# Kernel optimization log

Measured on AMD Instinct MI355X. Metric: run time of the kernel, lower is better.

Reference implementation:

```python
import jax, jax.numpy as jnp
import numpy as np

EPS = 1e-06


def setup_inputs() -> dict:
    key = jax.random.key(0)
    ks = jax.random.split(key, 8)
    B, N, D, r, T, O, Hid = 32, 2048, 64, 32, 31, 12, 128
    in_dim = r + T  # 63
    xav = lambda k, shape: jax.random.uniform(k, shape, jnp.float32, -1.0, 1.0) * np.sqrt(6.0 / (shape[0] + shape[1]))
    return {
        "H": jax.random.normal(ks[0], (B, N, D), jnp.float32),
        "ts_out": jax.random.uniform(ks[1], (B, O, T), jnp.float32),
        "O": O,
        "P_raw": xav(ks[2], (N, r)),
        "Q_raw": xav(ks[3], (N, r)),
        "W1": xav(ks[4], (in_dim, Hid)),
        "b1": jnp.zeros((Hid,), jnp.float32),
        "W2": xav(ks[5], (Hid, r)),
        "b2": jnp.zeros((r,), jnp.float32),
        "alpha": jax.random.uniform(ks[6], (1,), jnp.float32),
    }


def reference(H, ts_out, O, P_raw, Q_raw, W1, b1, W2, b2, alpha):
    # nonnegative_basis=True -> softplus on both bases
    P = jax.nn.softplus(P_raw)  # [N, r]
    Q = jax.nn.softplus(Q_raw)  # [N, r]
    # Right contraction: U = Q^T H per batch -> [B, r, D]
    U = jnp.einsum('bnd,nr->brd', H, Q)
    # Context norm over feature dim: [B, r]
    ctx = jnp.sqrt(jnp.mean(U * U, axis=-1) + EPS)
    # Gate features: concat([ts_out [B,O,T], ctx broadcast to [B,O,r]])
    B = H.shape[0]
    ctx_exp = jnp.broadcast_to(ctx[:, None, :], (B, O, ctx.shape[-1]))
    feat = jnp.concatenate([ts_out, ctx_exp], axis=-1)  # [B, O, T+r]
    # scale MLP with exact (erf) GELU, dropout=0 (eval)
    h = jax.nn.gelu(feat @ W1 + b1, approximate=False)
    s = jax.nn.softplus(h @ W2 + b2)  # [B, O, r]
    # M = P (s \odot U) without materializing NxN: [B, O, N, D]
    M = jnp.einsum('bor,brd,nr->bond', s, U, P)
    a = jnp.clip(alpha[0], 0.0, 1.0)
    H_base = H[:, None, :, :]  # broadcast over O
    H_graph = H_base + a * (M - H_base)
    return H_graph
```

## Files before the change

kernel.cpp:

```cpp
#include <hip/hip_runtime.h>
#include <math.h>

#define B_ 32
#define N_ 2048
#define D_ 64
#define R_ 32
#define T_ 31
#define O_ 12
#define HID_ 128
#define IN_DIM_ 63
#define NCH_ 32

#define OFF_QSP   0
#define OFF_UPART (OFF_QSP + N_*R_)
#define OFF_U     (OFF_UPART + B_*NCH_*R_*D_)
#define OFF_CTX   (OFF_U + B_*R_*D_)
#define OFF_PBF   (OFF_CTX + B_*R_)
#define OFF_SUT   (OFF_PBF + N_*R_/2)

typedef __attribute__((ext_vector_type(4))) float f32x4;
typedef __attribute__((ext_vector_type(8))) short short8;

__device__ __forceinline__ float softplus_f(float x) {
    return fmaxf(x, 0.0f) + log1pf(expf(-fabsf(x)));
}
__device__ __forceinline__ float gelu_f(float x) {
    return 0.5f * x * (1.0f + erff(x * 0.70710678118654752440f));
}
__device__ __forceinline__ unsigned short f2bf(float f) {
    unsigned int u = __float_as_uint(f);
    u = (u + 0x7FFFu + ((u >> 16) & 1u)) >> 16;
    return (unsigned short)u;
}

__global__ __launch_bounds__(256) void k_softplus(const float* __restrict__ Qr,
                                                  float* __restrict__ ws) {
    int i = blockIdx.x * blockDim.x + threadIdx.x;
    if (i < N_ * R_) ws[OFF_QSP + i] = softplus_f(Qr[i]);
}

__global__ __launch_bounds__(512) void k_upart(const float* __restrict__ H,
                                               const float* __restrict__ Pr,
                                               float* __restrict__ ws) {
    const float* __restrict__ Qsp = ws + OFF_QSP;
    float* __restrict__ Upart = ws + OFF_UPART;
    int b = blockIdx.x / NCH_;
    int c = blockIdx.x % NCH_;
    int tid = threadIdx.x;
    const int n0 = c * (N_ / NCH_);

    if (b == 0) {
        unsigned short* Pbf = (unsigned short*)(ws + OFF_PBF);
        #pragma unroll
        for (int i = tid; i < 64 * R_; i += 512)
            Pbf[(size_t)n0 * R_ + i] = f2bf(softplus_f(Pr[(size_t)n0 * R_ + i]));
    }

    int d = tid & 63;
    int rb = __builtin_amdgcn_readfirstlane(tid >> 6);
    const int r0 = rb * 4;
    float acc0 = 0.f, acc1 = 0.f, acc2 = 0.f, acc3 = 0.f;
    const float* __restrict__ Hb = H + ((size_t)b * N_ + n0) * D_ + d;
    #pragma unroll 2
    for (int i = 0; i < 64; ++i) {
        float h = Hb[(size_t)i * D_];
        const float* q = Qsp + (size_t)(n0 + i) * R_ + r0;
        acc0 = fmaf(h, q[0], acc0);
        acc1 = fmaf(h, q[1], acc1);
        acc2 = fmaf(h, q[2], acc2);
        acc3 = fmaf(h, q[3], acc3);
    }
    float* up = Upart + ((size_t)(b * NCH_ + c) * R_ + r0) * D_ + d;
    up[0 * D_] = acc0;
    up[1 * D_] = acc1;
    up[2 * D_] = acc2;
    up[3 * D_] = acc3;
}

__global__ __launch_bounds__(256) void k_ured(float* __restrict__ ws) {
    const float* __restrict__ Upart = ws + OFF_UPART;
    float* __restrict__ U = ws + OFF_U;
    float* __restrict__ ctx = ws + OFF_CTX;
    int b = blockIdx.x;
    int r = blockIdx.y * 4 + (threadIdx.x >> 6);
    int d = threadIdx.x & 63;
    float u = 0.f;
    #pragma unroll 8
    for (int c = 0; c < NCH_; ++c)
        u += Upart[((size_t)(b * NCH_ + c) * R_ + r) * D_ + d];
    U[((size_t)b * R_ + r) * D_ + d] = u;
    float sq = u * u;
    #pragma unroll
    for (int off = 32; off; off >>= 1) sq += __shfl_xor(sq, off, 64);
    if (d == 0) ctx[b * R_ + r] = sqrtf(sq * (1.0f / D_) + 1e-6f);
}

__global__ __launch_bounds__(128) void k_mlp(const float* __restrict__ ts_out,
                                             const float* __restrict__ W1,
                                             const float* __restrict__ b1,
                                             const float* __restrict__ W2,
                                             const float* __restrict__ b2,
                                             const float* __restrict__ alpha,
                                             float* __restrict__ ws) {
    __shared__ float feat[IN_DIM_];
    __shared__ float hsh[HID_];
    __shared__ float ssh[R_];
    int bo = blockIdx.x;
    int b = bo / O_;
    int tid = threadIdx.x;
    const float* __restrict__ ctx = ws + OFF_CTX;
    if (tid < T_) feat[tid] = ts_out[(size_t)bo * T_ + tid];
    else if (tid < IN_DIM_) feat[tid] = ctx[b * R_ + (tid - T_)];
    __syncthreads();
    float acc = b1[tid];
    #pragma unroll 9
    for (int k = 0; k < IN_DIM_; ++k) acc = fmaf(feat[k], W1[k * HID_ + tid], acc);
    hsh[tid] = gelu_f(acc);
    __syncthreads();
    if (tid < R_) {
        float a2 = b2[tid];
        #pragma unroll 8
        for (int j = 0; j < HID_; ++j) a2 = fmaf(hsh[j], W2[j * R_ + tid], a2);
        ssh[tid] = softplus_f(a2);
    }
    __syncthreads();
    float a = fminf(fmaxf(alpha[0], 0.0f), 1.0f);
    const float* __restrict__ U = ws + OFF_U;
    unsigned short* SUT = (unsigned short*)(ws + OFF_SUT) + (size_t)bo * D_ * R_;
    #pragma unroll
    for (int idx = tid; idx < D_ * R_; idx += 128) {
        int d = idx >> 5, r = idx & 31;
        SUT[idx] = f2bf(a * ssh[r] * U[((size_t)b * R_ + r) * D_ + d]);
    }
}

__global__ __launch_bounds__(256) void k_main(const float* __restrict__ H,
                                              const float* __restrict__ alpha,
                                              const float* __restrict__ ws,
                                              float* __restrict__ out) {
    __shared__ float tile[64 * 64];
    const int vid = blockIdx.x;
    const int b   = (vid & 7) * 4 + (vid >> 9);
    const int og  = (vid >> 8) & 1;
    const int nblk = ((vid >> 3) & 31) * 64;
    const int tid = threadIdx.x;
    const int w = tid >> 6;
    const int lane = tid & 63;
    const int l16 = lane & 15;
    const int lhi = lane >> 4;
    const int rl = w * 16 + l16;
    const float a = fminf(fmaxf(alpha[0], 0.0f), 1.0f);
    const float oma = 1.0f - a;

    const unsigned short* Pbf = (const unsigned short*)(ws + OFF_PBF);
    const unsigned short* SUT0 = (const unsigned short*)(ws + OFF_SUT)
                               + (size_t)(b * O_ + og * 6) * D_ * R_;

    short8 pfrag = *(const short8*)(Pbf + (size_t)(nblk + rl) * R_ + lhi * 8);

    const float* __restrict__ Hrow = H + ((size_t)b * N_ + nblk + rl) * D_;
    f32x4 homa[4];
    #pragma unroll
    for (int db = 0; db < 4; ++db)
        homa[db] = oma * *(const f32x4*)(Hrow + db * 16 + lhi * 4);

    char* tb = (char*)tile;
    float* __restrict__ oblk = out + ((size_t)(b * O_ + og * 6) * N_ + nblk) * D_;

    short8 sf[2][4];
    #pragma unroll
    for (int db = 0; db < 4; ++db)
        sf[0][db] = *(const short8*)(SUT0 + (size_t)(db * 16 + l16) * R_ + lhi * 8);
    #pragma unroll
    for (int oi = 0; oi < 6; ++oi) {
        const int cur = oi & 1, nxt = cur ^ 1;
        if (oi < 5) {
            const unsigned short* Sn = SUT0 + (size_t)(oi + 1) * D_ * R_;
            #pragma unroll
            for (int db = 0; db < 4; ++db)
                sf[nxt][db] = *(const short8*)(Sn + (size_t)(db * 16 + l16) * R_ + lhi * 8);
        }
        #pragma unroll
        for (int db = 0; db < 4; ++db) {
            f32x4 v = homa[db] + __builtin_amdgcn_mfma_f32_16x16x32_bf16(
                sf[cur][db], pfrag, (f32x4){0.f, 0.f, 0.f, 0.f}, 0, 0, 0);
            int c = (db * 64 + lhi * 16) ^ ((rl & 7) << 4);
            *(f32x4*)(tb + rl * 256 + c) = v;
        }
        char* op = (char*)(oblk + (size_t)oi * N_ * D_);
        #pragma unroll
        for (int i = 0; i < 4; ++i) {
            int g = w * 4096 + i * 1024 + lane * 16;
            int rr = g >> 8;
            int cc = (g & 255) ^ ((rr & 7) << 4);
            f32x4 v = *(const f32x4*)(tb + rr * 256 + cc);
            __builtin_nontemporal_store(v, (f32x4*)(op + g));
        }
    }
}

extern "C" void kernel_launch(void* const* d_in, const int* in_sizes, int n_in,
                              void* d_out, int out_size, void* d_ws, size_t ws_size,
                              hipStream_t stream) {
    const float* H      = (const float*)d_in[0];
    const float* ts_out = (const float*)d_in[1];
    const float* P_raw  = (const float*)d_in[3];
    const float* Q_raw  = (const float*)d_in[4];
    const float* W1     = (const float*)d_in[5];
    const float* b1     = (const float*)d_in[6];
    const float* W2     = (const float*)d_in[7];
    const float* b2     = (const float*)d_in[8];
    const float* alpha  = (const float*)d_in[9];
    float* out = (float*)d_out;
    float* ws  = (float*)d_ws;

    k_softplus<<<dim3((N_ * R_ + 255) / 256), dim3(256), 0, stream>>>(Q_raw, ws);
    k_upart<<<dim3(B_ * NCH_), dim3(512), 0, stream>>>(H, P_raw, ws);
    k_ured<<<dim3(B_, 8), dim3(256), 0, stream>>>(ws);
    k_mlp<<<dim3(B_ * O_), dim3(128), 0, stream>>>(ts_out, W1, b1, W2, b2, alpha, ws);
    k_main<<<dim3(2048), dim3(256), 0, stream>>>(H, alpha, ws, out);
}
```

Measured before the change: 73.99 us.

## Restructure main kernel to loop over N chunks per output slice with H/P prefetch

Each block of the main kernel now owns one (batch, output) pair and half the N range, holding its S·U fragments in registers. It loops over 16 row chunks, double-buffering the P and H loads in registers. Previously each block covered one 64-row tile and looped over 6 outputs, reusing H. The grid drops from 2048 to 768 blocks. The change trades H reuse across outputs (H is now re-read once per output) for fewer blocks and a longer pipelined streaming loop, at some cost in parallelism.

New measurement: 79.83 us. 7.9% more time.

```diff
diff --git a/kernel.cpp b/kernel.cpp
--- a/kernel.cpp
+++ b/kernel.cpp
@@ -140,9 +140,11 @@
                                               float* __restrict__ out) {
     __shared__ float tile[64 * 64];
     const int vid = blockIdx.x;
-    const int b   = (vid & 7) * 4 + (vid >> 9);
-    const int og  = (vid >> 8) & 1;
-    const int nblk = ((vid >> 3) & 31) * 64;
+    const int s   = vid >> 3;
+    const int b   = (vid & 7) * 4 + (s & 3);
+    const int q   = s >> 2;
+    const int o   = q >> 1;
+    const int nbase = (q & 1) * (N_ / 2);
     const int tid = threadIdx.x;
     const int w = tid >> 6;
     const int lane = tid & 63;
@@ -153,41 +155,42 @@
     const float oma = 1.0f - a;
 
     const unsigned short* Pbf = (const unsigned short*)(ws + OFF_PBF);
-    const unsigned short* SUT0 = (const unsigned short*)(ws + OFF_SUT)
-                               + (size_t)(b * O_ + og * 6) * D_ * R_;
-
-    short8 pfrag = *(const short8*)(Pbf + (size_t)(nblk + rl) * R_ + lhi * 8);
-
-    const float* __restrict__ Hrow = H + ((size_t)b * N_ + nblk + rl) * D_;
-    f32x4 homa[4];
+    const unsigned short* SUT = (const unsigned short*)(ws + OFF_SUT)
+                              + (size_t)(b * O_ + o) * D_ * R_;
+
+    short8 sf[4];
     #pragma unroll
     for (int db = 0; db < 4; ++db)
-        homa[db] = oma * *(const f32x4*)(Hrow + db * 16 + lhi * 4);
-
+        sf[db] = *(const short8*)(SUT + (size_t)(db * 16 + l16) * R_ + lhi * 8);
+
+    const float* __restrict__ Hb = H + ((size_t)b * N_ + nbase) * D_;
     char* tb = (char*)tile;
-    float* __restrict__ oblk = out + ((size_t)(b * O_ + og * 6) * N_ + nblk) * D_;
-
-    short8 sf[2][4];
+    char* __restrict__ outb = (char*)(out + ((size_t)(b * O_ + o) * N_ + nbase) * D_);
+
+    short8 pf[2];
+    f32x4 hv[2][4];
+    pf[0] = *(const short8*)(Pbf + (size_t)(nbase + rl) * R_ + lhi * 8);
     #pragma unroll
     for (int db = 0; db < 4; ++db)
-        sf[0][db] = *(const short8*)(SUT0 + (size_t)(db * 16 + l16) * R_ + lhi * 8);
-    #pragma unroll
-    for (int oi = 0; oi < 6; ++oi) {
-        const int cur = oi & 1, nxt = cur ^ 1;
-        if (oi < 5) {
-            const unsigned short* Sn = SUT0 + (size_t)(oi + 1) * D_ * R_;
+        hv[0][db] = *(const f32x4*)(Hb + (size_t)rl * D_ + db * 16 + lhi * 4);
+
+    for (int ch = 0; ch < 16; ++ch) {
+        const int cur = ch & 1, nxt = cur ^ 1;
+        if (ch < 15) {
+            const int rown = (ch + 1) * 64 + rl;
+            pf[nxt] = *(const short8*)(Pbf + (size_t)(nbase + rown) * R_ + lhi * 8);
             #pragma unroll
             for (int db = 0; db < 4; ++db)
-                sf[nxt][db] = *(const short8*)(Sn + (size_t)(db * 16 + l16) * R_ + lhi * 8);
+                hv[nxt][db] = *(const f32x4*)(Hb + (size_t)rown * D_ + db * 16 + lhi * 4);
         }
         #pragma unroll
         for (int db = 0; db < 4; ++db) {
-            f32x4 v = homa[db] + __builtin_amdgcn_mfma_f32_16x16x32_bf16(
-                sf[cur][db], pfrag, (f32x4){0.f, 0.f, 0.f, 0.f}, 0, 0, 0);
+            f32x4 v = oma * hv[cur][db] + __builtin_amdgcn_mfma_f32_16x16x32_bf16(
+                sf[db], pf[cur], (f32x4){0.f, 0.f, 0.f, 0.f}, 0, 0, 0);
             int c = (db * 64 + lhi * 16) ^ ((rl & 7) << 4);
             *(f32x4*)(tb + rl * 256 + c) = v;
         }
-        char* op = (char*)(oblk + (size_t)oi * N_ * D_);
+        char* op = outb + ch * 16384;
         #pragma unroll
         for (int i = 0; i < 4; ++i) {
             int g = w * 4096 + i * 1024 + lane * 16;
@@ -218,5 +221,5 @@
     k_upart<<<dim3(B_ * NCH_), dim3(512), 0, stream>>>(H, P_raw, ws);
     k_ured<<<dim3(B_, 8), dim3(256), 0, stream>>>(ws);
     k_mlp<<<dim3(B_ * O_), dim3(128), 0, stream>>>(ts_out, W1, b1, W2, b2, alpha, ws);
-    k_main<<<dim3(2048), dim3(256), 0, stream>>>(H, alpha, ws, out);
-}
+    k_main<<<dim3(768), dim3(256), 0, stream>>>(H, alpha, ws, out);
+}
```
